# Performance work log

Hardware: AMD Instinct MI355X
Metric: run time of the kernel (lower is better)

## Reference

```python
import jax, jax.numpy as jnp
import numpy as np

EPS = 1e-6
OMEGA = 0.1


def setup_inputs() -> dict:
    key = jax.random.key(0)
    k1, k2 = jax.random.split(key)
    n, d, kk = 4096, 128, 4
    inputs = jax.random.uniform(k1, (n, d), dtype=jnp.float32)  # positive so log(sim) is finite
    labels = jax.random.randint(k2, (n, kk), 0, 64, dtype=jnp.int64)
    return {"inputs": inputs, "labels": labels}


def reference(inputs, labels):
    n, kk = labels.shape
    sim = inputs @ inputs.T                      # [n, n]
    logsim = jnp.log(sim + EPS)                  # a_{jk} = log(sim[j,k]+eps)
    targets = labels[:, 0]
    eye = jnp.eye(n, dtype=bool)
    # pos_mask[j,k] = (targets[j] == targets[k]) xor diagonal
    pos = (targets[:, None] == targets[None, :]) & ~eye
    # eq[j,l,i] = (labels[l,i] == targets[j])
    eq = targets[:, None, None] == labels[None, :, :]
    m_idx = jnp.arange(kk)
    cols = kk - 1 - m_idx                        # neg_mask[m] uses label column kk-1-m
    # neg_mask[m][j,l] == 1  <=>  ~eq[j,l,kk-1-m]  AND  (m==0 or eq[j,l,kk-m])
    neq_col = ~eq[:, :, cols]                    # [j,l,m]
    prev_ok = jnp.concatenate(
        [jnp.ones((n, n, 1), dtype=bool), eq[:, :, cols[:-1]]], axis=-1)
    neg = neq_col & prev_ok                      # [j,l,m]
    # loss_pair[m] = log(Omega+eps) - log(Omega^(kk-m+1)+eps)
    lp = jnp.log(OMEGA + EPS) - jnp.log(OMEGA ** (kk - m_idx + 1) + EPS)  # [kk]
    dt = logsim.dtype
    posf = pos.astype(dt)
    negf = neg.astype(dt)
    # term = (a_jk - b_jlm)^2 with b_jlm = logsim[j,l] + 0.1*lp[m]
    # expand: sum_jklm pos*neg*(a^2 - 2ab + b^2), separable over k and (l,m)
    c = posf.sum(1)                              # [j] count of positives
    S1 = (posf * logsim).sum(1)                  # [j] sum a
    S2 = (posf * logsim ** 2).sum(1)             # [j] sum a^2
    b = logsim[:, :, None] + 0.1 * lp[None, None, :]   # [j,l,m]
    Ncnt = negf.sum(1)                           # [j,m]
    T1 = (negf * b).sum(1)                       # [j,m]
    T2 = (negf * b ** 2).sum(1)                  # [j,m]
    loss = (S2[:, None] * Ncnt - 2.0 * S1[:, None] * T1 + c[:, None] * T2).sum()
    return loss
```

## Files before the change

### kernel.cpp

```cpp
#include <hip/hip_runtime.h>
#include <math.h>

constexpr int N = 4096;
constexpr int D = 128;

constexpr size_t XBF_OFF = 0;
constexpr size_t TAB_OFF = (size_t)1 << 20;
constexpr size_t ACC_OFF = TAB_OFF + 64 * 4096;
constexpr size_t LSD_OFF = ACC_OFF + 5 * N * 4;
constexpr size_t SUM_OFF = LSD_OFF + N * 4;

typedef __attribute__((ext_vector_type(8))) short short8;
typedef __attribute__((ext_vector_type(4))) float floatx4;
typedef __attribute__((address_space(1))) unsigned int gu32;
typedef __attribute__((address_space(3))) unsigned int lu32;

__device__ inline unsigned f2bf(float f) {
  unsigned u = __builtin_bit_cast(unsigned, f);
  return (u + 0x7FFFu + ((u >> 16) & 1u)) >> 16;
}

__global__ __launch_bounds__(256) void k1_prep(
    const float* __restrict__ X, const int* __restrict__ labels,
    char* __restrict__ ws, float* __restrict__ out,
    float B0, float B1, float B2, float B3,
    float Q0, float Q1, float Q2, float Q3) {
  const int b = blockIdx.x, tid = threadIdx.x;
  if (b < 64) {
    const int t = b;
    __shared__ float red[4][4];
    unsigned char* tabu8 = (unsigned char*)(ws + TAB_OFF) + (size_t)t * N;
    float sg0 = 0.f, sgB = 0.f, sgQ = 0.f, ce0 = 0.f;
#pragma unroll 4
    for (int k = 0; k < 16; ++k) {
      const int j = k * 256 + tid;
      const int4 L = ((const int4*)labels)[j];
      const bool e0 = (t == L.x), e1 = (t == L.y), e2 = (t == L.z), e3 = (t == L.w);
      const bool n1 = e3 && !e2, n2 = e2 && !e1, n3 = e1 && !e0;
      sg0 += (e3 ? 0.f : 1.f) + (n1 ? 1.f : 0.f) + (n2 ? 1.f : 0.f) + (n3 ? 1.f : 0.f);
      sgB += (e3 ? 0.f : B0) + (n1 ? B1 : 0.f) + (n2 ? B2 : 0.f) + (n3 ? B3 : 0.f);
      sgQ += (e3 ? 0.f : Q0) + (n1 ? Q1 : 0.f) + (n2 ? Q2 : 0.f) + (n3 ? Q3 : 0.f);
      ce0 += e0 ? 1.f : 0.f;
      tabu8[j] = (unsigned char)((e1 ? 1u : 0u) | (e2 ? 2u : 0u) | (e3 ? 4u : 0u) | (e0 ? 8u : 0u));
    }
    const int w = tid >> 6, lane = tid & 63;
#pragma unroll
    for (int s = 1; s <= 32; s <<= 1) {
      sg0 += __shfl_xor(sg0, s, 64); sgB += __shfl_xor(sgB, s, 64);
      sgQ += __shfl_xor(sgQ, s, 64); ce0 += __shfl_xor(ce0, s, 64);
    }
    if (lane == 0) { red[w][0] = sg0; red[w][1] = sgB; red[w][2] = sgQ; red[w][3] = ce0; }
    __syncthreads();
    if (tid == 0) {
      float* sums = (float*)(ws + SUM_OFF);
      sums[t * 4 + 0] = red[0][0] + red[1][0] + red[2][0] + red[3][0];
      sums[t * 4 + 1] = red[0][1] + red[1][1] + red[2][1] + red[3][1];
      sums[t * 4 + 2] = red[0][2] + red[1][2] + red[2][2] + red[3][2];
      sums[t * 4 + 3] = red[0][3] + red[1][3] + red[2][3] + red[3][3];
    }
  } else if (b < 320) {
    const int task = (b - 64) * 256 + tid;
    const int r   = task >> 4;
    const int blk = task & 15;
    const float4 x0 = *(const float4*)&X[r * D + blk * 8];
    const float4 x1 = *(const float4*)&X[r * D + blk * 8 + 4];
    uint4 wv;
    wv.x = f2bf(x0.x) | (f2bf(x0.y) << 16);
    wv.y = f2bf(x0.z) | (f2bf(x0.w) << 16);
    wv.z = f2bf(x1.x) | (f2bf(x1.y) << 16);
    wv.w = f2bf(x1.z) | (f2bf(x1.w) << 16);
    *(uint4*)(ws + XBF_OFF + (size_t)r * 256 + ((blk ^ (r & 15)) * 16)) = wv;
  } else if (b < 336) {
    const int i = (b - 320) * 256 + tid;
    const float* xr = X + i * D;
    float s = 0.f;
#pragma unroll
    for (int c = 0; c < 32; ++c) {
      const float4 v = ((const float4*)xr)[c];
      s += v.x * v.x + v.y * v.y + v.z * v.z + v.w * v.w;
    }
    ((float*)(ws + LSD_OFF))[i] = __logf(s + 1e-6f);
  } else {
    const int idx = (b - 336) * 256 + tid;
    ((float*)(ws + ACC_OFF))[idx] = 0.f;
    if (idx == 0) out[0] = 0.f;
  }
}

__global__ __launch_bounds__(512, 4) void logratio_phaseA(
    const char* __restrict__ ws_ro, const int* __restrict__ labels,
    float* acc5, float B0, float B1, float B2, float B3) {

  __shared__ __align__(16) char smem[65792];

  const int tid  = threadIdx.x;
  const int w    = tid >> 6;
  const int lane = tid & 63;
  const int lc   = lane & 15;
  const int quad = lane >> 4;
  const int iBase = blockIdx.y * 128;
  const int jt0   = blockIdx.x * 4;

  float4* pal = (float4*)(smem + 65536);
  if (tid < 16) {
    const bool e1 = tid & 1, e2 = tid & 2, e3 = tid & 4, e0 = tid & 8;
    const bool n1 = e3 && !e2, n2 = e2 && !e1, n3 = e1 && !e0;
    const float g0 = (e3 ? 0.f : 1.f) + (n1 ? 1.f : 0.f) + (n2 ? 1.f : 0.f) + (n3 ? 1.f : 0.f);
    const float gB = (e3 ? 0.f : B0) + (n1 ? B1 : 0.f) + (n2 ? B2 : 0.f) + (n3 ? B3 : 0.f);
    pal[tid] = make_float4(gB, g0, e0 ? 1.f : 0.f, 0.f);
  }

  const char* xbf = ws_ro + XBF_OFF;
  {
    const char* gA_ = xbf + (size_t)iBase * 256 + w * 4096 + lane * 16;
#pragma unroll
    for (int c = 0; c < 4; ++c)
      __builtin_amdgcn_global_load_lds((const gu32*)(gA_ + c * 1024),
                                       (lu32*)(smem + 32768 + w * 4096 + c * 1024), 16, 0, 0);
  }
  const char* gBband = xbf + (size_t)jt0 * 128 * 256 + w * 4096 + lane * 16;
#pragma unroll
  for (int c = 0; c < 4; ++c)
    __builtin_amdgcn_global_load_lds((const gu32*)(gBband + c * 1024),
                                     (lu32*)(smem + w * 4096 + c * 1024), 16, 0, 0);

  int tis[4];
#pragma unroll
  for (int reg = 0; reg < 4; ++reg)
    tis[reg] = labels[(iBase + w * 16 + quad * 4 + reg) * 4];
  const unsigned char* tabu8 = (const unsigned char*)(ws_ro + TAB_OFF);
  const unsigned char* trow[4];
#pragma unroll
  for (int reg = 0; reg < 4; ++reg)
    trow[reg] = tabu8 + (size_t)tis[reg] * N + lc;

  float rU[4] = {}, rW[4] = {}, rV[4] = {}, rP1[4] = {}, rP2[4] = {};

  const char* Abase = smem + 32768 + (w * 16 + lc) * 256;
#pragma unroll 1
  for (int q = 0; q < 4; ++q) {
    __syncthreads();

    floatx4 acc[8] = {};
#pragma unroll
    for (int kb = 0; kb < 4; ++kb) {
      const int pb = ((kb * 4 + quad) ^ lc) * 16;
      const short8 af = *(const short8*)(Abase + pb);
      short8 bfr[8];
#pragma unroll
      for (int tn = 0; tn < 8; ++tn)
        bfr[tn] = *(const short8*)(smem + (tn * 16 + lc) * 256 + pb);
#pragma unroll
      for (int tn = 0; tn < 8; ++tn)
        acc[tn] = __builtin_amdgcn_mfma_f32_16x16x32_bf16(af, bfr[tn], acc[tn], 0, 0, 0);
    }
    __syncthreads();

    if (q < 3) {
      const char* g = gBband + (size_t)(q + 1) * 32768;
#pragma unroll
      for (int c = 0; c < 4; ++c)
        __builtin_amdgcn_global_load_lds((const gu32*)(g + c * 1024),
                                         (lu32*)(smem + w * 4096 + c * 1024), 16, 0, 0);
    }

    const int jBase = (jt0 + q) * 128;
#pragma unroll
    for (int reg = 0; reg < 4; ++reg) {
      const unsigned char* tr = trow[reg] + jBase;
#pragma unroll
      for (int tn = 0; tn < 8; ++tn) {
        const float4 pe = pal[tr[tn * 16]];
        const float ls = __logf(acc[tn][reg] + 1e-6f);
        const float u = pe.y * ls;
        rU[reg] += u;
        rW[reg] = fmaf(u, ls, rW[reg]);
        rV[reg] = fmaf(pe.x, ls, rV[reg]);
        const float p = pe.z * ls;
        rP1[reg] += p;
        rP2[reg] = fmaf(p, ls, rP2[reg]);
      }
    }
  }

  float* Red = (float*)smem;
#pragma unroll
  for (int reg = 0; reg < 4; ++reg) {
    float* dst = Red + (w * 16 + quad * 4 + reg) * 81 + lc * 5;
    dst[0] = rU[reg]; dst[1] = rW[reg]; dst[2] = rV[reg]; dst[3] = rP1[reg]; dst[4] = rP2[reg];
  }
  __syncthreads();

  if (tid < 128) {
    const int gi = iBase + tid;
    const float* src = Red + tid * 81;
    float s0 = 0.f, s1 = 0.f, s2 = 0.f, s3 = 0.f, s4 = 0.f;
#pragma unroll
    for (int l = 0; l < 16; ++l) {
      s0 += src[l * 5 + 0]; s1 += src[l * 5 + 1]; s2 += src[l * 5 + 2];
      s3 += src[l * 5 + 3]; s4 += src[l * 5 + 4];
    }
    atomicAdd(&acc5[0 * N + gi], s0);
    atomicAdd(&acc5[1 * N + gi], s1);
    atomicAdd(&acc5[2 * N + gi], s2);
    atomicAdd(&acc5[3 * N + gi], s3);
    atomicAdd(&acc5[4 * N + gi], s4);
  }
}

__global__ __launch_bounds__(256) void logratio_phaseB(
    const char* __restrict__ ws_ro, const int* __restrict__ labels,
    float* out) {
  const int i = blockIdx.x * 256 + threadIdx.x;
  const float* acc5 = (const float*)(ws_ro + ACC_OFF);
  const float U  = acc5[0 * N + i];
  const float W  = acc5[1 * N + i];
  const float V  = acc5[2 * N + i];
  const float P1 = acc5[3 * N + i];
  const float P2 = acc5[4 * N + i];
  const int t = labels[i * 4];
  const float4 S = ((const float4*)(ws_ro + SUM_OFF))[t];
  const float lsd = ((const float*)(ws_ro + LSD_OFF))[i];
  const float c  = S.w - 1.f;
  const float S1 = P1 - lsd;
  const float S2 = P2 - lsd * lsd;
  const float A  = S.x;
  const float Bv = U + S.y;
  const float Cv = W + 2.f * V + S.z;
  float v = S2 * A - 2.f * S1 * Bv + c * Cv;
#pragma unroll
  for (int m = 32; m >= 1; m >>= 1) v += __shfl_xor(v, m, 64);
  __shared__ float wsum[4];
  if ((threadIdx.x & 63) == 0) wsum[threadIdx.x >> 6] = v;
  __syncthreads();
  if (threadIdx.x == 0) atomicAdd(out, wsum[0] + wsum[1] + wsum[2] + wsum[3]);
}

extern "C" void kernel_launch(void* const* d_in, const int* in_sizes, int n_in,
                              void* d_out, int out_size, void* d_ws, size_t ws_size,
                              hipStream_t stream) {
  const float* inputs = (const float*)d_in[0];
  const int* labels = (const int*)d_in[1];
  float* out = (float*)d_out;
  char* ws = (char*)d_ws;

  float Bq[4], Qq[4];
  for (int m = 0; m < 4; ++m) {
    const float lpv = logf(0.1f + 1e-6f) - logf(powf(0.1f, (float)(5 - m)) + 1e-6f);
    Bq[m] = 0.1f * lpv;
    Qq[m] = Bq[m] * Bq[m];
  }

  k1_prep<<<416, 256, 0, stream>>>(inputs, labels, ws, out,
                                   Bq[0], Bq[1], Bq[2], Bq[3],
                                   Qq[0], Qq[1], Qq[2], Qq[3]);
  dim3 grid(8, 32);
  logratio_phaseA<<<grid, 512, 0, stream>>>(ws, labels, (float*)(ws + ACC_OFF),
                                            Bq[0], Bq[1], Bq[2], Bq[3]);
  logratio_phaseB<<<N / 256, 256, 0, stream>>>(ws, labels, out);
}
```

Before: 92.45 us.

## Split phaseA into one 128x128 tile per block with packed label table

Each block now handles a single 128x128 tile (grid 32x32) instead of looping over four column tiles, which cuts LDS to about 33KB and raises the occupancy hint to 8 blocks. A fragments are loaded straight from global memory into registers. The label-pattern table is repacked so each lane reads one 64-bit word holding its 8 patterns, instead of 8 scattered byte loads. The final reduction uses wave shuffles and per-row atomics in place of an LDS pass, at the cost of four times more blocks and more global atomics.

```diff
diff --git a/kernel.cpp b/kernel.cpp
--- a/kernel.cpp
+++ b/kernel.cpp
@@ -29,19 +29,27 @@
   if (b < 64) {
     const int t = b;
     __shared__ float red[4][4];
-    unsigned char* tabu8 = (unsigned char*)(ws + TAB_OFF) + (size_t)t * N;
+    unsigned long long* tabp = (unsigned long long*)(ws + TAB_OFF);
     float sg0 = 0.f, sgB = 0.f, sgQ = 0.f, ce0 = 0.f;
-#pragma unroll 4
-    for (int k = 0; k < 16; ++k) {
-      const int j = k * 256 + tid;
-      const int4 L = ((const int4*)labels)[j];
-      const bool e0 = (t == L.x), e1 = (t == L.y), e2 = (t == L.z), e3 = (t == L.w);
-      const bool n1 = e3 && !e2, n2 = e2 && !e1, n3 = e1 && !e0;
-      sg0 += (e3 ? 0.f : 1.f) + (n1 ? 1.f : 0.f) + (n2 ? 1.f : 0.f) + (n3 ? 1.f : 0.f);
-      sgB += (e3 ? 0.f : B0) + (n1 ? B1 : 0.f) + (n2 ? B2 : 0.f) + (n3 ? B3 : 0.f);
-      sgQ += (e3 ? 0.f : Q0) + (n1 ? Q1 : 0.f) + (n2 ? Q2 : 0.f) + (n3 ? Q3 : 0.f);
-      ce0 += e0 ? 1.f : 0.f;
-      tabu8[j] = (unsigned char)((e1 ? 1u : 0u) | (e2 ? 2u : 0u) | (e3 ? 4u : 0u) | (e0 ? 8u : 0u));
+#pragma unroll 2
+    for (int it = 0; it < 2; ++it) {
+      const int pr = it * 256 + tid;
+      const int jb = pr >> 4, lcc = pr & 15;
+      unsigned long long pk = 0ull;
+#pragma unroll
+      for (int tn = 0; tn < 8; ++tn) {
+        const int j = jb * 128 + tn * 16 + lcc;
+        const int4 L = ((const int4*)labels)[j];
+        const bool e0 = (t == L.x), e1 = (t == L.y), e2 = (t == L.z), e3 = (t == L.w);
+        const bool n1 = e3 && !e2, n2 = e2 && !e1, n3 = e1 && !e0;
+        sg0 += (e3 ? 0.f : 1.f) + (n1 ? 1.f : 0.f) + (n2 ? 1.f : 0.f) + (n3 ? 1.f : 0.f);
+        sgB += (e3 ? 0.f : B0) + (n1 ? B1 : 0.f) + (n2 ? B2 : 0.f) + (n3 ? B3 : 0.f);
+        sgQ += (e3 ? 0.f : Q0) + (n1 ? Q1 : 0.f) + (n2 ? Q2 : 0.f) + (n3 ? Q3 : 0.f);
+        ce0 += e0 ? 1.f : 0.f;
+        const unsigned long long p = (e1 ? 1u : 0u) | (e2 ? 2u : 0u) | (e3 ? 4u : 0u) | (e0 ? 8u : 0u);
+        pk |= p << (8 * tn);
+      }
+      tabp[((size_t)t * 32 + jb) * 16 + lcc] = pk;
     }
     const int w = tid >> 6, lane = tid & 63;
 #pragma unroll
@@ -87,21 +95,22 @@
   }
 }
 
-__global__ __launch_bounds__(512, 4) void logratio_phaseA(
+__global__ __launch_bounds__(512, 8) void logratio_phaseA(
     const char* __restrict__ ws_ro, const int* __restrict__ labels,
     float* acc5, float B0, float B1, float B2, float B3) {
 
-  __shared__ __align__(16) char smem[65792];
+  __shared__ __align__(16) char smem[33024];
 
   const int tid  = threadIdx.x;
   const int w    = tid >> 6;
   const int lane = tid & 63;
   const int lc   = lane & 15;
   const int quad = lane >> 4;
+  const int jb   = blockIdx.x;
+  const int jBase = jb * 128;
   const int iBase = blockIdx.y * 128;
-  const int jt0   = blockIdx.x * 4;
-
-  float4* pal = (float4*)(smem + 65536);
+
+  float4* pal = (float4*)(smem + 32768);
   if (tid < 16) {
     const bool e1 = tid & 1, e2 = tid & 2, e3 = tid & 4, e0 = tid & 8;
     const bool n1 = e3 && !e2, n2 = e2 && !e1, n3 = e1 && !e0;
@@ -112,99 +121,80 @@
 
   const char* xbf = ws_ro + XBF_OFF;
   {
-    const char* gA_ = xbf + (size_t)iBase * 256 + w * 4096 + lane * 16;
+    const char* gB_ = xbf + (size_t)jBase * 256 + w * 4096 + lane * 16;
 #pragma unroll
     for (int c = 0; c < 4; ++c)
-      __builtin_amdgcn_global_load_lds((const gu32*)(gA_ + c * 1024),
-                                       (lu32*)(smem + 32768 + w * 4096 + c * 1024), 16, 0, 0);
-  }
-  const char* gBband = xbf + (size_t)jt0 * 128 * 256 + w * 4096 + lane * 16;
-#pragma unroll
-  for (int c = 0; c < 4; ++c)
-    __builtin_amdgcn_global_load_lds((const gu32*)(gBband + c * 1024),
-                                     (lu32*)(smem + w * 4096 + c * 1024), 16, 0, 0);
-
+      __builtin_amdgcn_global_load_lds((const gu32*)(gB_ + c * 1024),
+                                       (lu32*)(smem + w * 4096 + c * 1024), 16, 0, 0);
+  }
+  short8 af[4];
+  {
+    const char* arow = xbf + (size_t)(iBase + w * 16 + lc) * 256;
+#pragma unroll
+    for (int kb = 0; kb < 4; ++kb)
+      af[kb] = *(const short8*)(arow + (((kb * 4 + quad) ^ lc) * 16));
+  }
   int tis[4];
 #pragma unroll
   for (int reg = 0; reg < 4; ++reg)
     tis[reg] = labels[(iBase + w * 16 + quad * 4 + reg) * 4];
-  const unsigned char* tabu8 = (const unsigned char*)(ws_ro + TAB_OFF);
-  const unsigned char* trow[4];
+  const unsigned long long* tabp = (const unsigned long long*)(ws_ro + TAB_OFF);
+  unsigned long long tpk[4];
 #pragma unroll
   for (int reg = 0; reg < 4; ++reg)
-    trow[reg] = tabu8 + (size_t)tis[reg] * N + lc;
+    tpk[reg] = tabp[((size_t)tis[reg] * 32 + jb) * 16 + lc];
+
+  __syncthreads();
+
+  floatx4 acc[8] = {};
+#pragma unroll
+  for (int kb = 0; kb < 4; ++kb) {
+    const int pb = ((kb * 4 + quad) ^ lc) * 16;
+    short8 bfr[8];
+#pragma unroll
+    for (int tn = 0; tn < 8; ++tn)
+      bfr[tn] = *(const short8*)(smem + (tn * 16 + lc) * 256 + pb);
+#pragma unroll
+    for (int tn = 0; tn < 8; ++tn)
+      acc[tn] = __builtin_amdgcn_mfma_f32_16x16x32_bf16(af[kb], bfr[tn], acc[tn], 0, 0, 0);
+  }
 
   float rU[4] = {}, rW[4] = {}, rV[4] = {}, rP1[4] = {}, rP2[4] = {};
-
-  const char* Abase = smem + 32768 + (w * 16 + lc) * 256;
-#pragma unroll 1
-  for (int q = 0; q < 4; ++q) {
-    __syncthreads();
-
-    floatx4 acc[8] = {};
-#pragma unroll
-    for (int kb = 0; kb < 4; ++kb) {
-      const int pb = ((kb * 4 + quad) ^ lc) * 16;
-      const short8 af = *(const short8*)(Abase + pb);
-      short8 bfr[8];
-#pragma unroll
-      for (int tn = 0; tn < 8; ++tn)
-        bfr[tn] = *(const short8*)(smem + (tn * 16 + lc) * 256 + pb);
-#pragma unroll
-      for (int tn = 0; tn < 8; ++tn)
-        acc[tn] = __builtin_amdgcn_mfma_f32_16x16x32_bf16(af, bfr[tn], acc[tn], 0, 0, 0);
-    }
-    __syncthreads();
-
-    if (q < 3) {
-      const char* g = gBband + (size_t)(q + 1) * 32768;
-#pragma unroll
-      for (int c = 0; c < 4; ++c)
-        __builtin_amdgcn_global_load_lds((const gu32*)(g + c * 1024),
-                                         (lu32*)(smem + w * 4096 + c * 1024), 16, 0, 0);
-    }
-
-    const int jBase = (jt0 + q) * 128;
-#pragma unroll
-    for (int reg = 0; reg < 4; ++reg) {
-      const unsigned char* tr = trow[reg] + jBase;
-#pragma unroll
-      for (int tn = 0; tn < 8; ++tn) {
-        const float4 pe = pal[tr[tn * 16]];
-        const float ls = __logf(acc[tn][reg] + 1e-6f);
-        const float u = pe.y * ls;
-        rU[reg] += u;
-        rW[reg] = fmaf(u, ls, rW[reg]);
-        rV[reg] = fmaf(pe.x, ls, rV[reg]);
-        const float p = pe.z * ls;
-        rP1[reg] += p;
-        rP2[reg] = fmaf(p, ls, rP2[reg]);
-      }
-    }
-  }
-
-  float* Red = (float*)smem;
 #pragma unroll
   for (int reg = 0; reg < 4; ++reg) {
-    float* dst = Red + (w * 16 + quad * 4 + reg) * 81 + lc * 5;
-    dst[0] = rU[reg]; dst[1] = rW[reg]; dst[2] = rV[reg]; dst[3] = rP1[reg]; dst[4] = rP2[reg];
-  }
-  __syncthreads();
-
-  if (tid < 128) {
-    const int gi = iBase + tid;
-    const float* src = Red + tid * 81;
-    float s0 = 0.f, s1 = 0.f, s2 = 0.f, s3 = 0.f, s4 = 0.f;
-#pragma unroll
-    for (int l = 0; l < 16; ++l) {
-      s0 += src[l * 5 + 0]; s1 += src[l * 5 + 1]; s2 += src[l * 5 + 2];
-      s3 += src[l * 5 + 3]; s4 += src[l * 5 + 4];
-    }
-    atomicAdd(&acc5[0 * N + gi], s0);
-    atomicAdd(&acc5[1 * N + gi], s1);
-    atomicAdd(&acc5[2 * N + gi], s2);
-    atomicAdd(&acc5[3 * N + gi], s3);
-    atomicAdd(&acc5[4 * N + gi], s4);
+    const unsigned long long pk = tpk[reg];
+#pragma unroll
+    for (int tn = 0; tn < 8; ++tn) {
+      const unsigned pat = (unsigned)(pk >> (8 * tn)) & 15u;
+      const float4 pe = pal[pat];
+      const float ls = __logf(acc[tn][reg] + 1e-6f);
+      const float u = pe.y * ls;
+      rU[reg] += u;
+      rW[reg] = fmaf(u, ls, rW[reg]);
+      rV[reg] = fmaf(pe.x, ls, rV[reg]);
+      const float p = pe.z * ls;
+      rP1[reg] += p;
+      rP2[reg] = fmaf(p, ls, rP2[reg]);
+    }
+  }
+
+#pragma unroll
+  for (int reg = 0; reg < 4; ++reg) {
+    float s0 = rU[reg], s1 = rW[reg], s2 = rV[reg], s3 = rP1[reg], s4 = rP2[reg];
+#pragma unroll
+    for (int m = 1; m <= 8; m <<= 1) {
+      s0 += __shfl_xor(s0, m, 64); s1 += __shfl_xor(s1, m, 64);
+      s2 += __shfl_xor(s2, m, 64); s3 += __shfl_xor(s3, m, 64);
+      s4 += __shfl_xor(s4, m, 64);
+    }
+    if (lc == 0) {
+      const int gi = iBase + w * 16 + quad * 4 + reg;
+      atomicAdd(&acc5[0 * N + gi], s0);
+      atomicAdd(&acc5[1 * N + gi], s1);
+      atomicAdd(&acc5[2 * N + gi], s2);
+      atomicAdd(&acc5[3 * N + gi], s3);
+      atomicAdd(&acc5[4 * N + gi], s4);
+    }
   }
 }
 
@@ -254,7 +244,7 @@
   k1_prep<<<416, 256, 0, stream>>>(inputs, labels, ws, out,
                                    Bq[0], Bq[1], Bq[2], Bq[3],
                                    Qq[0], Qq[1], Qq[2], Qq[3]);
-  dim3 grid(8, 32);
+  dim3 grid(N / 128, N / 128);
   logratio_phaseA<<<grid, 512, 0, stream>>>(ws, labels, (float*)(ws + ACC_OFF),
                                             Bq[0], Bq[1], Bq[2], Bq[3]);
   logratio_phaseB<<<N / 256, 256, 0, stream>>>(ws, labels, out);
```

After: 163.6 us. 76.9% more time.
